# Kernel tuning notes

Hardware: AMD Instinct MI355X
Metric: run time of the kernel (lower is better)

The kernel has to match this reference:

```python
import jax, jax.numpy as jnp
import numpy as np
from jax import lax

SEQ, BATCH, IN, HID, OUT = 28, 8192, 28, 128, 10


def _lstm_layer(x, W_ih, W_hh, b_ih, b_hh):
    # x: [T, B, in]; PyTorch gate order: i, f, g, o
    # precompute input projection once (keeps scan body memory-bound on h only)
    xproj = jnp.einsum('tbi,gi->tbg', x, W_ih) + b_ih + b_hh  # [T, B, 4H]
    H = W_hh.shape[1]
    B = x.shape[1]
    h0 = jnp.zeros((B, H), x.dtype)
    c0 = jnp.zeros((B, H), x.dtype)

    def step(carry, xp_t):
        h, c = carry
        gates = xp_t + h @ W_hh.T  # [B, 4H]
        i, f, g, o = jnp.split(gates, 4, axis=-1)
        i = jax.nn.sigmoid(i)
        f = jax.nn.sigmoid(f)
        g = jnp.tanh(g)
        o = jax.nn.sigmoid(o)
        c = f * c + i * g
        h = o * jnp.tanh(c)
        return (h, c), h

    _, ys = lax.scan(step, (h0, c0), xproj)
    return ys  # [T, B, H]


def setup_inputs() -> dict:
    key = jax.random.key(0)
    ks = jax.random.split(key, 11)
    s_in = 1.0 / np.sqrt(HID)
    u = lambda k, shape: jax.random.uniform(k, shape, jnp.float32, -s_in, s_in)
    return {
        'X': jax.random.normal(ks[0], (SEQ, BATCH, IN), jnp.float32),
        'W_ih0': u(ks[1], (4 * HID, IN)),
        'W_hh0': u(ks[2], (4 * HID, HID)),
        'b_ih0': u(ks[3], (4 * HID,)),
        'b_hh0': u(ks[4], (4 * HID,)),
        'W_ih1': u(ks[5], (4 * HID, HID)),
        'W_hh1': u(ks[6], (4 * HID, HID)),
        'b_ih1': u(ks[7], (4 * HID,)),
        'b_hh1': u(ks[8], (4 * HID,)),
        'W_lin': u(ks[9], (OUT, HID)),
        'b_lin': u(ks[10], (OUT,)),
    }


def reference(X, W_ih0, W_hh0, b_ih0, b_hh0, W_ih1, W_hh1, b_ih1, b_hh1, W_lin, b_lin):
    h1 = _lstm_layer(X, W_ih0, W_hh0, b_ih0, b_hh0)   # [T, B, 128]
    h2 = _lstm_layer(h1, W_ih1, W_hh1, b_ih1, b_hh1)  # [T, B, 128]
    pred = h2[-1] @ W_lin.T + b_lin                   # [B, 10]
    return pred
```

## Files before the change

kernel.cpp:

```cpp
#include <hip/hip_runtime.h>
#include <hip/hip_bf16.h>

#define SEQ   28
#define BATCH 8192
#define NIN   28
#define HID   128
#define NOUT  10

#define SCL_SIG  (-1.4426950408889634f)
#define SCL_TANH (2.8853900817779268f)

typedef __bf16 bf16_t;
typedef __bf16 bf16x8 __attribute__((ext_vector_type(8)));
typedef float  f32x4  __attribute__((ext_vector_type(4)));

__device__ __forceinline__ unsigned swz(unsigned row, unsigned byte_in_row) {
    return row * 256u + (byte_in_row ^ ((row & 7u) << 4));
}

__global__ void pack_w_kernel(const float* __restrict__ Whh0, bf16_t* __restrict__ o0,
                              const float* __restrict__ Whh1, bf16_t* __restrict__ o1,
                              const float* __restrict__ Wih1, bf16_t* __restrict__ o2) {
    int idx = blockIdx.x * 256 + threadIdx.x;
    int mi = idx >> 16;
    int e  = idx & 65535;
    const float* W = (mi == 0) ? Whh0 : (mi == 1) ? Whh1 : Wih1;
    bf16_t*      o = (mi == 0) ? o0   : (mi == 1) ? o1   : o2;
    int j    = e & 7;
    int frag = e >> 3;
    int lane = frag & 63;
    int ksnt = frag >> 6;
    int nt = ksnt & 31, ks = ksnt >> 5;
    int gate = nt * 16 + (lane & 15);
    int k    = ks * 32 + ((lane >> 4) << 3) + j;
    float s  = ((gate >> 7) == 2) ? SCL_TANH : SCL_SIG;
    o[e] = (bf16_t)(W[gate * 128 + k] * s);
}

template <int LAYER>
__device__ __forceinline__ void lstm_step(
    int t, int rb, int tid, int lane, int w, int l15, int l4,
    unsigned char* smem,
    const float* __restrict__ X, const bf16_t* __restrict__ h1r,
    bf16_t* __restrict__ h1w,
    bf16x8 (&whh)[4][4], bf16x8 (&wih)[4][4],
    float (&bias)[4], float (&c)[2][4], bf16x8 (&x)[4][2])
{
    constexpr int KS = (LAYER == 0) ? 1 : 4;
    unsigned char* hb = smem + ((t & 1) << 13);
    unsigned char* hn = smem + ((~t & 1) << 13);

    bf16x8 ah[4][2];
    #pragma unroll
    for (int ks = 0; ks < 4; ++ks)
        #pragma unroll
        for (int m = 0; m < 2; ++m)
            ah[ks][m] = *(const bf16x8*)(hb + swz(16 * m + l15, (ks * 32 + l4 * 8) * 2));

    f32x4 acc[2][4];
    #pragma unroll
    for (int m = 0; m < 2; ++m)
        #pragma unroll
        for (int q = 0; q < 4; ++q) {
            f32x4 b = {bias[q], bias[q], bias[q], bias[q]};
            acc[m][q] = b;
        }

    #pragma unroll
    for (int m = 0; m < 2; ++m)
        #pragma unroll
        for (int q = 0; q < 4; ++q)
            #pragma unroll
            for (int ks = 0; ks < KS; ++ks)
                acc[m][q] = __builtin_amdgcn_mfma_f32_16x16x32_bf16(
                    x[ks][m], wih[q][ks], acc[m][q], 0, 0, 0);

    if (t + 1 < SEQ) {
        if constexpr (LAYER == 0) {
            #pragma unroll
            for (int m = 0; m < 2; ++m) {
                const float* base = X + ((size_t)((t + 1) * BATCH + rb + 16 * m + l15)) * NIN + l4 * 8;
                f32x4 lo = *(const f32x4*)base;
                f32x4 hi = {0.f, 0.f, 0.f, 0.f};
                if (l4 < 3) hi = *(const f32x4*)(base + 4);
                bf16x8 v;
                #pragma unroll
                for (int j = 0; j < 4; ++j) { v[j] = (bf16_t)lo[j]; v[4 + j] = (bf16_t)hi[j]; }
                x[0][m] = v;
            }
        } else {
            #pragma unroll
            for (int ks = 0; ks < 4; ++ks)
                #pragma unroll
                for (int m = 0; m < 2; ++m)
                    x[ks][m] = *(const bf16x8*)(h1r + ((size_t)((t + 1) * BATCH + rb + 16 * m + l15)) * HID + ks * 32 + l4 * 8);
        }
    }

    #pragma unroll
    for (int m = 0; m < 2; ++m)
        #pragma unroll
        for (int q = 0; q < 4; ++q)
            #pragma unroll
            for (int ks = 0; ks < 4; ++ks)
                acc[m][q] = __builtin_amdgcn_mfma_f32_16x16x32_bf16(
                    ah[ks][m], whh[q][ks], acc[m][q], 0, 0, 0);

    #pragma unroll
    for (int m = 0; m < 2; ++m)
        #pragma unroll
        for (int r = 0; r < 4; ++r) {
            float Ei = __builtin_amdgcn_exp2f(acc[m][0][r]);
            float Ef = __builtin_amdgcn_exp2f(acc[m][1][r]);
            float Eg = __builtin_amdgcn_exp2f(acc[m][2][r]);
            float Eo = __builtin_amdgcn_exp2f(acc[m][3][r]);
            float ti = 1.0f + Ei, tf = 1.0f + Ef;
            float tg = 1.0f + Eg, to = 1.0f + Eo;
            float gt  = fmaf(-2.0f, __builtin_amdgcn_rcpf(tg), 1.0f);
            float rif = __builtin_amdgcn_rcpf(tf * ti);
            float cn  = fmaf(c[m][r], ti, gt * tf) * rif;
            c[m][r] = cn;
            float Ec = __builtin_amdgcn_exp2f(SCL_TANH * cn);
            float hv = (Ec - 1.0f) * __builtin_amdgcn_rcpf(to * (1.0f + Ec));
            *(bf16_t*)(hn + swz(16 * m + l4 * 4 + r, (16 * w + l15) * 2)) = (bf16_t)hv;
        }
    __syncthreads();

    if constexpr (LAYER == 0) {
        int row = tid >> 4, sc = tid & 15;
        f32x4 v = *(const f32x4*)(hn + swz(row, sc * 16));
        *(f32x4*)((unsigned char*)h1w + ((size_t)(t * BATCH + rb + row)) * 256 + sc * 16) = v;
    }
}

__global__ __launch_bounds__(512, 2)
void lstm_fused_kernel(const float* __restrict__ Wih0,
                       const float* __restrict__ bih0, const float* __restrict__ bhh0,
                       const float* __restrict__ bih1, const float* __restrict__ bhh1,
                       const float* __restrict__ X,
                       const bf16_t* __restrict__ whhp0,
                       const bf16_t* __restrict__ whhp1,
                       const bf16_t* __restrict__ wihp1,
                       bf16_t* __restrict__ h1,
                       const float* __restrict__ Wlin, const float* __restrict__ blin,
                       float* __restrict__ out)
{
    __shared__ unsigned char smem[16384] __attribute__((aligned(16)));

    const int tid  = threadIdx.x;
    const int lane = tid & 63;
    const int w    = tid >> 6;
    const int l15  = lane & 15;
    const int l4   = lane >> 4;
    const int rb   = blockIdx.x * 32;

    bf16x8 whh[4][4], wih[4][4];
    float  bias[4];
    float  c[2][4];
    bf16x8 x[4][2];

    #pragma unroll
    for (int q = 0; q < 4; ++q)
        #pragma unroll
        for (int ks = 0; ks < 4; ++ks)
            whh[q][ks] = *(const bf16x8*)(whhp0 + ((size_t)((ks * 32 + (w + 8 * q)) * 64 + lane)) * 8);
    #pragma unroll
    for (int q = 0; q < 4; ++q) {
        int gate = 16 * w + 128 * q + l15;
        float s = (q == 2) ? SCL_TANH : SCL_SIG;
        #pragma unroll
        for (int j = 0; j < 8; ++j) {
            int k = l4 * 8 + j;
            wih[q][0][j] = (k < NIN) ? (bf16_t)(Wih0[gate * NIN + k] * s) : (bf16_t)0.0f;
        }
        bias[q] = (bih0[gate] + bhh0[gate]) * s;
        c[0][q] = 0.f; c[1][q] = 0.f;
    }
    for (int i = tid * 16; i < 16384; i += 512 * 16) {
        f32x4 z = {0.f, 0.f, 0.f, 0.f};
        *(f32x4*)(smem + i) = z;
    }
    #pragma unroll
    for (int m = 0; m < 2; ++m) {
        const float* base = X + ((size_t)(rb + 16 * m + l15)) * NIN + l4 * 8;
        f32x4 lo = *(const f32x4*)base;
        f32x4 hi = {0.f, 0.f, 0.f, 0.f};
        if (l4 < 3) hi = *(const f32x4*)(base + 4);
        bf16x8 v;
        #pragma unroll
        for (int j = 0; j < 4; ++j) { v[j] = (bf16_t)lo[j]; v[4 + j] = (bf16_t)hi[j]; }
        x[0][m] = v;
    }
    __syncthreads();

    for (int t = 0; t < SEQ; ++t)
        lstm_step<0>(t, rb, tid, lane, w, l15, l4, smem, X, nullptr, h1,
                     whh, wih, bias, c, x);

    __syncthreads();

    #pragma unroll
    for (int q = 0; q < 4; ++q) {
        #pragma unroll
        for (int ks = 0; ks < 4; ++ks) {
            whh[q][ks] = *(const bf16x8*)(whhp1 + ((size_t)((ks * 32 + (w + 8 * q)) * 64 + lane)) * 8);
            wih[q][ks] = *(const bf16x8*)(wihp1 + ((size_t)((ks * 32 + (w + 8 * q)) * 64 + lane)) * 8);
        }
        int gate = 16 * w + 128 * q + l15;
        float s = (q == 2) ? SCL_TANH : SCL_SIG;
        bias[q] = (bih1[gate] + bhh1[gate]) * s;
        c[0][q] = 0.f; c[1][q] = 0.f;
    }
    for (int i = tid * 16; i < 16384; i += 512 * 16) {
        f32x4 z = {0.f, 0.f, 0.f, 0.f};
        *(f32x4*)(smem + i) = z;
    }
    #pragma unroll
    for (int ks = 0; ks < 4; ++ks)
        #pragma unroll
        for (int m = 0; m < 2; ++m)
            x[ks][m] = *(const bf16x8*)(h1 + ((size_t)(rb + 16 * m + l15)) * HID + ks * 32 + l4 * 8);
    __syncthreads();

    for (int t = 0; t < SEQ; ++t)
        lstm_step<1>(t, rb, tid, lane, w, l15, l4, smem, nullptr, h1, nullptr,
                     whh, wih, bias, c, x);

    if (tid < 32 * NOUT) {
        int row = tid / NOUT, oc = tid % NOUT;
        const unsigned char* hf = smem;
        float s = blin[oc];
        #pragma unroll 8
        for (int k = 0; k < HID; ++k) {
            float h = (float)*(const bf16_t*)(hf + swz(row, k * 2));
            s += h * Wlin[oc * HID + k];
        }
        out[(size_t)(rb + row) * NOUT + oc] = s;
    }
}

extern "C" void kernel_launch(void* const* d_in, const int* in_sizes, int n_in,
                              void* d_out, int out_size, void* d_ws, size_t ws_size,
                              hipStream_t stream) {
    const float* X    = (const float*)d_in[0];
    const float* Wih0 = (const float*)d_in[1];
    const float* Whh0 = (const float*)d_in[2];
    const float* bih0 = (const float*)d_in[3];
    const float* bhh0 = (const float*)d_in[4];
    const float* Wih1 = (const float*)d_in[5];
    const float* Whh1 = (const float*)d_in[6];
    const float* bih1 = (const float*)d_in[7];
    const float* bhh1 = (const float*)d_in[8];
    const float* Wlin = (const float*)d_in[9];
    const float* blin = (const float*)d_in[10];
    float* out = (float*)d_out;
    (void)Wih1;

    unsigned char* ws = (unsigned char*)d_ws;
    bf16_t* h1    = (bf16_t*)(ws);
    bf16_t* whhp0 = (bf16_t*)(ws + 58720256);
    bf16_t* whhp1 = (bf16_t*)(ws + 58851328);
    bf16_t* wihp1 = (bf16_t*)(ws + 58982400);

    pack_w_kernel<<<dim3(768), dim3(256), 0, stream>>>(Whh0, whhp0, Whh1, whhp1, Wih1, wihp1);

    lstm_fused_kernel<<<dim3(256), dim3(512), 0, stream>>>(
        Wih0, bih0, bhh0, bih1, bhh1, X, whhp0, whhp1, wihp1, h1,
        Wlin, blin, out);
}
```

Measured before the change: 131.7 us.

## Prefetch layer-0 inputs two steps ahead, trim barrier and gate math

Layer 0 now double-buffers the x input registers (xA/xB) and loads inputs two timesteps ahead, so global load latency has a full extra step to hide. The __syncthreads at the end of each step is replaced by an inline-asm barrier that waits only on LDS counters (lgkmcnt), so outstanding global loads are not drained at the barrier. The cell-state update is reformulated to use one reciprocal instead of two. The cost is more live vector registers for the second x buffer, with a risk to occupancy under launch_bounds(512,2). Layer 1 keeps a one-step prefetch through the same interface.

```diff
diff --git a/kernel.cpp b/kernel.cpp
--- a/kernel.cpp
+++ b/kernel.cpp
@@ -16,6 +16,10 @@
 
 __device__ __forceinline__ unsigned swz(unsigned row, unsigned byte_in_row) {
     return row * 256u + (byte_in_row ^ ((row & 7u) << 4));
+}
+
+__device__ __forceinline__ void barrier_lds() {
+    asm volatile("s_waitcnt lgkmcnt(0)\n\ts_barrier" ::: "memory");
 }
 
 __global__ void pack_w_kernel(const float* __restrict__ Whh0, bf16_t* __restrict__ o0,
@@ -37,14 +41,27 @@
     o[e] = (bf16_t)(W[gate * 128 + k] * s);
 }
 
+__device__ __forceinline__ bf16x8 load_x0(const float* __restrict__ X,
+                                          int t, int rb, int m, int l15, int l4) {
+    const float* base = X + ((size_t)(t * BATCH + rb + 16 * m + l15)) * NIN + l4 * 8;
+    f32x4 lo = *(const f32x4*)base;
+    f32x4 hi = {0.f, 0.f, 0.f, 0.f};
+    if (l4 < 3) hi = *(const f32x4*)(base + 4);
+    bf16x8 v;
+    #pragma unroll
+    for (int j = 0; j < 4; ++j) { v[j] = (bf16_t)lo[j]; v[4 + j] = (bf16_t)hi[j]; }
+    return v;
+}
+
 template <int LAYER>
 __device__ __forceinline__ void lstm_step(
-    int t, int rb, int tid, int lane, int w, int l15, int l4,
+    int t, int tload, int rb, int tid, int lane, int w, int l15, int l4,
     unsigned char* smem,
     const float* __restrict__ X, const bf16_t* __restrict__ h1r,
     bf16_t* __restrict__ h1w,
     bf16x8 (&whh)[4][4], bf16x8 (&wih)[4][4],
-    float (&bias)[4], float (&c)[2][4], bf16x8 (&x)[4][2])
+    float (&bias)[4], float (&c)[2][4],
+    bf16x8 (&xc)[4][2], bf16x8 (&xl)[4][2])
 {
     constexpr int KS = (LAYER == 0) ? 1 : 4;
     unsigned char* hb = smem + ((t & 1) << 13);
@@ -73,27 +90,19 @@
             #pragma unroll
             for (int ks = 0; ks < KS; ++ks)
                 acc[m][q] = __builtin_amdgcn_mfma_f32_16x16x32_bf16(
-                    x[ks][m], wih[q][ks], acc[m][q], 0, 0, 0);
-
-    if (t + 1 < SEQ) {
+                    xc[ks][m], wih[q][ks], acc[m][q], 0, 0, 0);
+
+    if (tload < SEQ) {
         if constexpr (LAYER == 0) {
             #pragma unroll
-            for (int m = 0; m < 2; ++m) {
-                const float* base = X + ((size_t)((t + 1) * BATCH + rb + 16 * m + l15)) * NIN + l4 * 8;
-                f32x4 lo = *(const f32x4*)base;
-                f32x4 hi = {0.f, 0.f, 0.f, 0.f};
-                if (l4 < 3) hi = *(const f32x4*)(base + 4);
-                bf16x8 v;
-                #pragma unroll
-                for (int j = 0; j < 4; ++j) { v[j] = (bf16_t)lo[j]; v[4 + j] = (bf16_t)hi[j]; }
-                x[0][m] = v;
-            }
+            for (int m = 0; m < 2; ++m)
+                xl[0][m] = load_x0(X, tload, rb, m, l15, l4);
         } else {
             #pragma unroll
             for (int ks = 0; ks < 4; ++ks)
                 #pragma unroll
                 for (int m = 0; m < 2; ++m)
-                    x[ks][m] = *(const bf16x8*)(h1r + ((size_t)((t + 1) * BATCH + rb + 16 * m + l15)) * HID + ks * 32 + l4 * 8);
+                    xl[ks][m] = *(const bf16x8*)(h1r + ((size_t)(tload * BATCH + rb + 16 * m + l15)) * HID + ks * 32 + l4 * 8);
         }
     }
 
@@ -116,15 +125,15 @@
             float Eo = __builtin_amdgcn_exp2f(acc[m][3][r]);
             float ti = 1.0f + Ei, tf = 1.0f + Ef;
             float tg = 1.0f + Eg, to = 1.0f + Eo;
-            float gt  = fmaf(-2.0f, __builtin_amdgcn_rcpf(tg), 1.0f);
-            float rif = __builtin_amdgcn_rcpf(tf * ti);
-            float cn  = fmaf(c[m][r], ti, gt * tf) * rif;
+            float titg = ti * tg;
+            float num  = fmaf(c[m][r], titg, tf * (tg - 2.0f));
+            float cn   = num * __builtin_amdgcn_rcpf(tf * titg);
             c[m][r] = cn;
             float Ec = __builtin_amdgcn_exp2f(SCL_TANH * cn);
             float hv = (Ec - 1.0f) * __builtin_amdgcn_rcpf(to * (1.0f + Ec));
             *(bf16_t*)(hn + swz(16 * m + l4 * 4 + r, (16 * w + l15) * 2)) = (bf16_t)hv;
         }
-    __syncthreads();
+    barrier_lds();
 
     if constexpr (LAYER == 0) {
         int row = tid >> 4, sc = tid & 15;
@@ -157,7 +166,7 @@
     bf16x8 whh[4][4], wih[4][4];
     float  bias[4];
     float  c[2][4];
-    bf16x8 x[4][2];
+    bf16x8 xA[4][2], xB[4][2];
 
     #pragma unroll
     for (int q = 0; q < 4; ++q)
@@ -182,20 +191,17 @@
     }
     #pragma unroll
     for (int m = 0; m < 2; ++m) {
-        const float* base = X + ((size_t)(rb + 16 * m + l15)) * NIN + l4 * 8;
-        f32x4 lo = *(const f32x4*)base;
-        f32x4 hi = {0.f, 0.f, 0.f, 0.f};
-        if (l4 < 3) hi = *(const f32x4*)(base + 4);
-        bf16x8 v;
-        #pragma unroll
-        for (int j = 0; j < 4; ++j) { v[j] = (bf16_t)lo[j]; v[4 + j] = (bf16_t)hi[j]; }
-        x[0][m] = v;
+        xA[0][m] = load_x0(X, 0, rb, m, l15, l4);
+        xB[0][m] = load_x0(X, 1, rb, m, l15, l4);
     }
     __syncthreads();
 
-    for (int t = 0; t < SEQ; ++t)
-        lstm_step<0>(t, rb, tid, lane, w, l15, l4, smem, X, nullptr, h1,
-                     whh, wih, bias, c, x);
+    for (int t = 0; t < SEQ; t += 2) {
+        lstm_step<0>(t,     t + 2, rb, tid, lane, w, l15, l4, smem, X, nullptr, h1,
+                     whh, wih, bias, c, xA, xA);
+        lstm_step<0>(t + 1, t + 3, rb, tid, lane, w, l15, l4, smem, X, nullptr, h1,
+                     whh, wih, bias, c, xB, xB);
+    }
 
     __syncthreads();
 
@@ -219,12 +225,12 @@
     for (int ks = 0; ks < 4; ++ks)
         #pragma unroll
         for (int m = 0; m < 2; ++m)
-            x[ks][m] = *(const bf16x8*)(h1 + ((size_t)(rb + 16 * m + l15)) * HID + ks * 32 + l4 * 8);
+            xA[ks][m] = *(const bf16x8*)(h1 + ((size_t)(rb + 16 * m + l15)) * HID + ks * 32 + l4 * 8);
     __syncthreads();
 
     for (int t = 0; t < SEQ; ++t)
-        lstm_step<1>(t, rb, tid, lane, w, l15, l4, smem, nullptr, h1, nullptr,
-                     whh, wih, bias, c, x);
+        lstm_step<1>(t, t + 1, rb, tid, lane, w, l15, l4, smem, nullptr, h1, nullptr,
+                     whh, wih, bias, c, xA, xA);
 
     if (tid < 32 * NOUT) {
         int row = tid / NOUT, oc = tid % NOUT;
@@ -254,7 +260,6 @@
     const float* Wlin = (const float*)d_in[9];
     const float* blin = (const float*)d_in[10];
     float* out = (float*)d_out;
-    (void)Wih1;
 
     unsigned char* ws = (unsigned char*)d_ws;
     bf16_t* h1    = (bf16_t*)(ws);
```

Result: no change. 133.1 us (+1.1%).
